# Performance work log

Measured on AMD Instinct MI355X. Metric: run time of the kernel, lower is better.

## Reference

```python
import jax, jax.numpy as jnp
import numpy as np

D_MODEL = 1024
D_FF = 2048
NA = 4
NB = 4
E = NA * NB
B = 2
S = 1024


def setup_inputs() -> dict:
    key = jax.random.key(0)
    ks = jax.random.split(key, 8)
    s = 0.02
    x = jax.random.normal(ks[0], (B, S, D_MODEL), dtype=jnp.float32)
    # stacked per-expert FFN params (torch Linear stored as [in, out] here)
    W1 = (jax.random.normal(ks[1], (E, D_MODEL, 2 * D_FF), dtype=jnp.float32) * s)
    b1 = jnp.zeros((E, 2 * D_FF), dtype=jnp.float32)
    W2 = (jax.random.normal(ks[2], (E, D_FF, D_MODEL), dtype=jnp.float32) * s)
    b2 = jnp.zeros((E, D_MODEL), dtype=jnp.float32)
    Wga = jax.random.normal(ks[3], (D_MODEL, NA), dtype=jnp.float32) * s
    bga = jnp.zeros((NA,), dtype=jnp.float32)
    Wgb = jax.random.normal(ks[4], (D_MODEL, NB), dtype=jnp.float32) * s
    bgb = jnp.zeros((NB,), dtype=jnp.float32)
    return {"x": x, "W1": W1, "b1": b1, "W2": W2, "b2": b2,
            "Wga": Wga, "bga": bga, "Wgb": Wgb, "bgb": bgb}


def reference(x, W1, b1, W2, b2, Wga, bga, Wgb, bgb):
    b, s, d = x.shape
    xf = x.reshape(b * s, d)                     # [T, d]
    probs_A = jax.nn.softmax(xf @ Wga + bga, axis=-1)   # [T, NA]
    probs_B = jax.nn.softmax(xf @ Wgb + bgb, axis=-1)   # [T, NB]
    idx_A = jnp.argmax(probs_A, axis=-1)
    idx_B = jnp.argmax(probs_B, axis=-1)
    oh_A = jax.nn.one_hot(idx_A, NA, dtype=xf.dtype)
    oh_B = jax.nn.one_hot(idx_B, NB, dtype=xf.dtype)
    aux_A = NA * jnp.sum(probs_A.mean(0) * oh_A.mean(0))
    aux_B = NB * jnp.sum(probs_B.mean(0) * oh_B.mean(0))
    total_aux = aux_A + aux_B

    # flattened Cartesian expert index per token
    e_idx = idx_A * NB + idx_B                   # [T]

    # run all experts densely, then select per token (vectorized dispatch)
    h = jnp.einsum('td,edf->etf', xf, W1) + b1[:, None, :]   # [E, T, 2*d_ff]
    a, g = jnp.split(h, 2, axis=-1)
    act = a * jax.nn.silu(g)                                  # [E, T, d_ff]
    y = jnp.einsum('etf,efd->etd', act, W2) + b2[:, None, :]  # [E, T, d]
    oh_E = jax.nn.one_hot(e_idx, E, dtype=xf.dtype)           # [T, E]
    out = jnp.einsum('te,etd->td', oh_E, y)                   # [T, d]
    return out.reshape(b, s, d), total_aux
```

## Files before the change

### kernel.cpp

```cpp
#include <hip/hip_runtime.h>
#include <cstdint>
#include <cstddef>

#define TOKENS 2048
#define DM 1024
#define DFF 2048
#define HC 4096
#define NE 16
#define BM 256

typedef __bf16 bf16x8 __attribute__((ext_vector_type(8)));
typedef float floatx4 __attribute__((ext_vector_type(4)));

static __device__ __forceinline__ unsigned short f2bf(float f) {
    union { float f; unsigned int u; } v; v.f = f;
    unsigned int r = v.u + 0x7fffu + ((v.u >> 16) & 1u);
    return (unsigned short)(r >> 16);
}

static __device__ __forceinline__ void lds_barrier() {
    asm volatile("s_waitcnt lgkmcnt(0)" ::: "memory");
    __builtin_amdgcn_s_barrier();
    __builtin_amdgcn_sched_barrier(0);
}

__global__ __launch_bounds__(256) void moe_gating(
    const float* __restrict__ x, const float* __restrict__ Wga, const float* __restrict__ bga,
    const float* __restrict__ Wgb, const float* __restrict__ bgb,
    float* __restrict__ probsA, float* __restrict__ probsB, int* __restrict__ e_idx)
{
    int wv = threadIdx.x >> 6, lane = threadIdx.x & 63;
    int t = blockIdx.x * 4 + wv;
    const float* xr = x + (size_t)t * DM;
    double aA[4] = {0.,0.,0.,0.}, aB[4] = {0.,0.,0.,0.};
    for (int k = lane; k < DM; k += 64) {
        double xv = (double)xr[k];
        float4 wa = *(const float4*)(Wga + k * 4);
        float4 wb = *(const float4*)(Wgb + k * 4);
        aA[0] += xv * wa.x; aA[1] += xv * wa.y; aA[2] += xv * wa.z; aA[3] += xv * wa.w;
        aB[0] += xv * wb.x; aB[1] += xv * wb.y; aB[2] += xv * wb.z; aB[3] += xv * wb.w;
    }
    #pragma unroll
    for (int off = 32; off >= 1; off >>= 1) {
        #pragma unroll
        for (int j = 0; j < 4; ++j) {
            aA[j] += __shfl_xor(aA[j], off);
            aB[j] += __shfl_xor(aB[j], off);
        }
    }
    if (lane == 0) {
        double lA[4], lB[4];
        #pragma unroll
        for (int j = 0; j < 4; ++j) {
            lA[j] = aA[j] + (double)bga[j];
            lB[j] = aB[j] + (double)bgb[j];
        }
        int ia = 0, ib = 0;
        #pragma unroll
        for (int j = 1; j < 4; ++j) {
            if (lA[j] > lA[ia]) ia = j;
            if (lB[j] > lB[ib]) ib = j;
        }
        double sA = 0., sB = 0., pA[4], pB[4];
        #pragma unroll
        for (int j = 0; j < 4; ++j) {
            pA[j] = exp(lA[j] - lA[ia]); sA += pA[j];
            pB[j] = exp(lB[j] - lB[ib]); sB += pB[j];
        }
        float4 oa, ob;
        oa.x = (float)(pA[0]/sA); oa.y = (float)(pA[1]/sA);
        oa.z = (float)(pA[2]/sA); oa.w = (float)(pA[3]/sA);
        ob.x = (float)(pB[0]/sB); ob.y = (float)(pB[1]/sB);
        ob.z = (float)(pB[2]/sB); ob.w = (float)(pB[3]/sB);
        *(float4*)(probsA + t * 4) = oa;
        *(float4*)(probsB + t * 4) = ob;
        e_idx[t] = ia * 4 + ib;
    }
}

__global__ __launch_bounds__(256) void moe_stats(
    const float* __restrict__ probsA, const float* __restrict__ probsB,
    const int* __restrict__ e_idx,
    int* __restrict__ countE, int* __restrict__ offsets, float* __restrict__ aux_out)
{
    __shared__ float sA[4], sB[4];
    __shared__ int cA[4], cB[4], cE[16];
    int tid = threadIdx.x;
    if (tid < 4) { sA[tid] = 0.f; sB[tid] = 0.f; cA[tid] = 0; cB[tid] = 0; }
    if (tid < 16) cE[tid] = 0;
    __syncthreads();
    float lA[4] = {0,0,0,0}, lB[4] = {0,0,0,0};
    for (int t = tid; t < TOKENS; t += 256) {
        float4 pa = *(const float4*)(probsA + t * 4);
        float4 pb = *(const float4*)(probsB + t * 4);
        lA[0] += pa.x; lA[1] += pa.y; lA[2] += pa.z; lA[3] += pa.w;
        lB[0] += pb.x; lB[1] += pb.y; lB[2] += pb.z; lB[3] += pb.w;
        int e = e_idx[t];
        atomicAdd(&cE[e], 1);
        atomicAdd(&cA[e >> 2], 1);
        atomicAdd(&cB[e & 3], 1);
    }
    #pragma unroll
    for (int j = 0; j < 4; ++j) {
        atomicAdd(&sA[j], lA[j]);
        atomicAdd(&sB[j], lB[j]);
    }
    __syncthreads();
    if (tid == 0) {
        int acc = 0;
        for (int e = 0; e < NE; ++e) { offsets[e] = acc; countE[e] = cE[e]; acc += cE[e]; }
        offsets[NE] = acc;
        float invT = 1.0f / (float)TOKENS;
        float auxA = 0.f, auxB = 0.f;
        for (int j = 0; j < 4; ++j) {
            auxA += (sA[j] * invT) * ((float)cA[j] * invT);
            auxB += (sB[j] * invT) * ((float)cB[j] * invT);
        }
        aux_out[0] = 4.0f * auxA + 4.0f * auxB;
    }
}

__global__ __launch_bounds__(256) void moe_slot(const int* __restrict__ e_idx,
                                                const int* __restrict__ offsets,
                                                int* __restrict__ cursor, int* __restrict__ perm)
{
    int t = blockIdx.x * 256 + threadIdx.x;
    int e = e_idx[t];
    int s = offsets[e] + atomicAdd(&cursor[e], 1);
    perm[s] = t;
}

__global__ __launch_bounds__(256) void moe_gather(const float* __restrict__ x,
                                                  const int* __restrict__ perm,
                                                  unsigned short* __restrict__ Xg)
{
    int s = blockIdx.x;
    int t = perm[s];
    int i = threadIdx.x * 4;
    float4 v = *(const float4*)(x + (size_t)t * DM + i);
    ushort4 o;
    o.x = f2bf(v.x); o.y = f2bf(v.y); o.z = f2bf(v.z); o.w = f2bf(v.w);
    *(ushort4*)(Xg + (size_t)s * DM + i) = o;
}

__global__ __launch_bounds__(512) void moe_ffn1(
    const unsigned short* __restrict__ Xg, const float* __restrict__ W1,
    const float* __restrict__ b1, const int* __restrict__ countE,
    const int* __restrict__ offsets, unsigned short* __restrict__ actbuf)
{
    int e = blockIdx.y;
    int cnt = countE[e];
    if (cnt == 0) return;
    int base = offsets[e];
    int n0 = blockIdx.x * 64;
    __shared__ __align__(16) unsigned short Xs[2 * BM * 40];
    int tid = threadIdx.x, wv = tid >> 6, lane = tid & 63;
    int quad = lane >> 4, l15 = lane & 15;
    int wvM = wv >> 2, wvN = wv & 3;
    const float* W1e = W1 + (size_t)e * DM * HC;
    int col = n0 + wvN * 16 + l15;
    const float* pa = W1e + col;
    const float* pg = W1e + DFF + col;
    float ba = b1[e * HC + col];
    float bg = b1[e * HC + DFF + col];
    int row = tid >> 2, kc = tid & 3;

    for (int m0 = 0; m0 < cnt; m0 += BM) {
        floatx4 acc[8][2];
        #pragma unroll
        for (int i = 0; i < 8; ++i) {
            acc[i][0] = floatx4{0.f,0.f,0.f,0.f};
            acc[i][1] = floatx4{0.f,0.f,0.f,0.f};
        }
        {
            uint4 av0 = {0u,0u,0u,0u}, av1 = {0u,0u,0u,0u};
            int ma = m0 + row, mb = m0 + row + 128;
            if (ma < cnt) av0 = *(const uint4*)(Xg + (size_t)(base + ma) * DM + kc * 8);
            if (mb < cnt) av1 = *(const uint4*)(Xg + (size_t)(base + mb) * DM + kc * 8);
            *(uint4*)(Xs + row * 40 + kc * 8) = av0;
            *(uint4*)(Xs + (row + 128) * 40 + kc * 8) = av1;
        }
        float curA[8], curG[8], nxtA[8], nxtG[8];
        {
            const float* qa = pa + (size_t)(quad * 8) * HC;
            const float* qg = pg + (size_t)(quad * 8) * HC;
            #pragma unroll
            for (int j = 0; j < 8; ++j) { curA[j] = qa[(size_t)j * HC]; curG[j] = qg[(size_t)j * HC]; }
        }
        lds_barrier();
        for (int ks = 0; ks < DM / 32; ++ks) {
            int buf = ks & 1;
            uint4 nv0 = {0u,0u,0u,0u}, nv1 = {0u,0u,0u,0u};
            bool more = (ks + 1 < DM / 32);
            if (more) {
                int k0n = (ks + 1) * 32;
                int ma = m0 + row, mb = m0 + row + 128;
                if (ma < cnt) nv0 = *(const uint4*)(Xg + (size_t)(base + ma) * DM + k0n + kc * 8);
                if (mb < cnt) nv1 = *(const uint4*)(Xg + (size_t)(base + mb) * DM + k0n + kc * 8);
                const float* qa = pa + (size_t)((ks + 1) * 32 + quad * 8) * HC;
                const float* qg = pg + (size_t)((ks + 1) * 32 + quad * 8) * HC;
                #pragma unroll
                for (int j = 0; j < 8; ++j) { nxtA[j] = qa[(size_t)j * HC]; nxtG[j] = qg[(size_t)j * HC]; }
            }
            bf16x8 af[8];
            #pragma unroll
            for (int i = 0; i < 8; ++i)
                af[i] = *(const bf16x8*)(Xs + buf * (BM * 40) + (wvM * 128 + i * 16 + l15) * 40 + quad * 8);
            bf16x8 fa, fg;
            #pragma unroll
            for (int j = 0; j < 8; ++j) { fa[j] = (__bf16)curA[j]; fg[j] = (__bf16)curG[j]; }
            #pragma unroll
            for (int i = 0; i < 8; ++i) {
                acc[i][0] = __builtin_amdgcn_mfma_f32_16x16x32_bf16(af[i], fa, acc[i][0], 0, 0, 0);
                acc[i][1] = __builtin_amdgcn_mfma_f32_16x16x32_bf16(af[i], fg, acc[i][1], 0, 0, 0);
            }
            if (more) {
                *(uint4*)(Xs + (buf ^ 1) * (BM * 40) + row * 40 + kc * 8) = nv0;
                *(uint4*)(Xs + (buf ^ 1) * (BM * 40) + (row + 128) * 40 + kc * 8) = nv1;
                #pragma unroll
                for (int j = 0; j < 8; ++j) { curA[j] = nxtA[j]; curG[j] = nxtG[j]; }
            }
            lds_barrier();
        }
        #pragma unroll
        for (int i = 0; i < 8; ++i) {
            #pragma unroll
            for (int r = 0; r < 4; ++r) {
                int mr = m0 + wvM * 128 + i * 16 + quad * 4 + r;
                if (mr < cnt) {
                    float a = acc[i][0][r] + ba;
                    float g = acc[i][1][r] + bg;
                    float sg = 1.0f / (1.0f + __expf(-g));
                    actbuf[(size_t)(base + mr) * DFF + col] = f2bf(a * (g * sg));
                }
            }
        }
    }
}

__global__ __launch_bounds__(512) void moe_ffn2(
    const unsigned short* __restrict__ actbuf, const float* __restrict__ W2,
    const float* __restrict__ b2, const int* __restrict__ countE,
    const int* __restrict__ offsets, const int* __restrict__ perm,
    float* __restrict__ out)
{
    int e = blockIdx.y;
    int cnt = countE[e];
    if (cnt == 0) return;
    int base = offsets[e];
    int n0 = blockIdx.x * 64;
    __shared__ __align__(16) unsigned short As[2 * BM * 40];
    int tid = threadIdx.x, wv = tid >> 6, lane = tid & 63;
    int quad = lane >> 4, l15 = lane & 15;
    int wvM = wv >> 2, wvN = wv & 3;
    const float* W2e = W2 + (size_t)e * DFF * DM;
    int col = n0 + wvN * 16 + l15;
    const float* pb = W2e + col;
    float bias = b2[e * DM + col];
    int row = tid >> 2, kc = tid & 3;

    for (int m0 = 0; m0 < cnt; m0 += BM) {
        floatx4 acc[8];
        #pragma unroll
        for (int i = 0; i < 8; ++i) acc[i] = floatx4{0.f,0.f,0.f,0.f};
        {
            uint4 av0 = {0u,0u,0u,0u}, av1 = {0u,0u,0u,0u};
            int ma = m0 + row, mb = m0 + row + 128;
            if (ma < cnt) av0 = *(const uint4*)(actbuf + (size_t)(base + ma) * DFF + kc * 8);
            if (mb < cnt) av1 = *(const uint4*)(actbuf + (size_t)(base + mb) * DFF + kc * 8);
            *(uint4*)(As + row * 40 + kc * 8) = av0;
            *(uint4*)(As + (row + 128) * 40 + kc * 8) = av1;
        }
        float curB[8], nxtB[8];
        {
            const float* qb = pb + (size_t)(quad * 8) * DM;
            #pragma unroll
            for (int j = 0; j < 8; ++j) curB[j] = qb[(size_t)j * DM];
        }
        lds_barrier();
        for (int ks = 0; ks < DFF / 32; ++ks) {
            int buf = ks & 1;
            uint4 nv0 = {0u,0u,0u,0u}, nv1 = {0u,0u,0u,0u};
            bool more = (ks + 1 < DFF / 32);
            if (more) {
                int k0n = (ks + 1) * 32;
                int ma = m0 + row, mb = m0 + row + 128;
                if (ma < cnt) nv0 = *(const uint4*)(actbuf + (size_t)(base + ma) * DFF + k0n + kc * 8);
                if (mb < cnt) nv1 = *(const uint4*)(actbuf + (size_t)(base + mb) * DFF + k0n + kc * 8);
                const float* qb = pb + (size_t)((ks + 1) * 32 + quad * 8) * DM;
                #pragma unroll
                for (int j = 0; j < 8; ++j) nxtB[j] = qb[(size_t)j * DM];
            }
            bf16x8 af[8];
            #pragma unroll
            for (int i = 0; i < 8; ++i)
                af[i] = *(const bf16x8*)(As + buf * (BM * 40) + (wvM * 128 + i * 16 + l15) * 40 + quad * 8);
            bf16x8 fb;
            #pragma unroll
            for (int j = 0; j < 8; ++j) fb[j] = (__bf16)curB[j];
            #pragma unroll
            for (int i = 0; i < 8; ++i)
                acc[i] = __builtin_amdgcn_mfma_f32_16x16x32_bf16(af[i], fb, acc[i], 0, 0, 0);
            if (more) {
                *(uint4*)(As + (buf ^ 1) * (BM * 40) + row * 40 + kc * 8) = nv0;
                *(uint4*)(As + (buf ^ 1) * (BM * 40) + (row + 128) * 40 + kc * 8) = nv1;
                #pragma unroll
                for (int j = 0; j < 8; ++j) curB[j] = nxtB[j];
            }
            lds_barrier();
        }
        #pragma unroll
        for (int i = 0; i < 8; ++i) {
            #pragma unroll
            for (int r = 0; r < 4; ++r) {
                int mr = m0 + wvM * 128 + i * 16 + quad * 4 + r;
                if (mr < cnt) {
                    int t = perm[base + mr];
                    out[(size_t)t * DM + col] = acc[i][r] + bias;
                }
            }
        }
    }
}

extern "C" void kernel_launch(void* const* d_in, const int* in_sizes, int n_in,
                              void* d_out, int out_size, void* d_ws, size_t ws_size,
                              hipStream_t stream)
{
    (void)in_sizes; (void)n_in; (void)out_size; (void)ws_size;
    const float* x   = (const float*)d_in[0];
    const float* W1  = (const float*)d_in[1];
    const float* b1  = (const float*)d_in[2];
    const float* W2  = (const float*)d_in[3];
    const float* b2  = (const float*)d_in[4];
    const float* Wga = (const float*)d_in[5];
    const float* bga = (const float*)d_in[6];
    const float* Wgb = (const float*)d_in[7];
    const float* bgb = (const float*)d_in[8];
    float* out = (float*)d_out;

    char* ws = (char*)d_ws;
    int*   countE  = (int*)(ws + 0);
    int*   cursor  = (int*)(ws + 64);
    int*   offsets = (int*)(ws + 256);
    int*   e_idx   = (int*)(ws + 512);
    int*   perm    = (int*)(ws + 8704);
    float* probsA  = (float*)(ws + 16896);
    float* probsB  = (float*)(ws + 49664);
    unsigned short* Xg     = (unsigned short*)(ws + 131072);
    unsigned short* actbuf = (unsigned short*)(ws + (size_t)8 * 1024 * 1024);

    hipMemsetAsync(ws, 0, 256, stream);
    moe_gating<<<TOKENS / 4, 256, 0, stream>>>(x, Wga, bga, Wgb, bgb,
                                               probsA, probsB, e_idx);
    moe_stats<<<1, 256, 0, stream>>>(probsA, probsB, e_idx, countE, offsets,
                                     out + (size_t)TOKENS * DM);
    moe_slot<<<TOKENS / 256, 256, 0, stream>>>(e_idx, offsets, cursor, perm);
    moe_gather<<<TOKENS, 256, 0, stream>>>(x, perm, Xg);
    moe_ffn1<<<dim3(DFF / 64, NE), 512, 0, stream>>>(Xg, W1, b1, countE, offsets, actbuf);
    moe_ffn2<<<dim3(DM / 64, NE), 512, 0, stream>>>(actbuf, W2, b2, countE, offsets, perm, out);
}
```

Baseline: 535.7 us.

## Retile expert FFN GEMMs to 192-row tiles with deeper A-prefetch and block swizzle

Both expert GEMM kernels now run 256-thread blocks, where each wave owns a 16-column strip and covers all 192 rows. Before, 512 threads split 256 rows across two wave groups. A activations are prefetched two k-steps ahead through register double buffers in an unrolled pair-step macro, and block IDs are remapped with an 8-way interleave that spreads experts across XCDs. The aim is fewer M-tiles for expert counts near 128 tokens, better latency hiding and occupancy of two blocks per CU. The cost is more accumulators per thread and higher register pressure.

```diff
diff --git a/kernel.cpp b/kernel.cpp
--- a/kernel.cpp
+++ b/kernel.cpp
@@ -7,7 +7,9 @@
 #define DFF 2048
 #define HC 4096
 #define NE 16
-#define BM 256
+#define BM 192
+#define NBX1 32
+#define NBX2 16
 
 typedef __bf16 bf16x8 __attribute__((ext_vector_type(8)));
 typedef float floatx4 __attribute__((ext_vector_type(4)));
@@ -143,22 +145,63 @@
     *(ushort4*)(Xg + (size_t)s * DM + i) = o;
 }
 
-__global__ __launch_bounds__(512) void moe_ffn1(
+#define NS1 (DM / 32)
+
+#define FFN1_STEP(ksv, RW, RL) {                                               \
+    int buf_ = (ksv) & 1;                                                      \
+    if ((ksv) + 1 < NS1) {                                                     \
+        _Pragma("unroll")                                                      \
+        for (int p = 0; p < 3; ++p)                                            \
+            *(uint4*)(Xs + (buf_ ^ 1) * (BM * 40) + (row + p * 64) * 40 + kc * 8) = RW[p]; \
+    }                                                                          \
+    if ((ksv) + 2 < NS1) {                                                     \
+        int k0n_ = ((ksv) + 2) * 32;                                           \
+        _Pragma("unroll")                                                      \
+        for (int p = 0; p < 3; ++p) {                                          \
+            int m_ = m0 + row + p * 64;                                        \
+            RL[p].x = 0u; RL[p].y = 0u; RL[p].z = 0u; RL[p].w = 0u;            \
+            if (m_ < cnt) RL[p] = *(const uint4*)(Xg + (size_t)(base + m_) * DM + k0n_ + kc * 8); \
+        }                                                                      \
+    }                                                                          \
+    if ((ksv) + 1 < NS1) {                                                     \
+        const float* qa_ = pa + (size_t)(((ksv) + 1) * 32 + quad * 8) * HC;    \
+        const float* qg_ = pg + (size_t)(((ksv) + 1) * 32 + quad * 8) * HC;    \
+        _Pragma("unroll")                                                      \
+        for (int j = 0; j < 8; ++j) { nxtA[j] = qa_[(size_t)j * HC]; nxtG[j] = qg_[(size_t)j * HC]; } \
+    }                                                                          \
+    bf16x8 fa_, fg_;                                                           \
+    _Pragma("unroll")                                                          \
+    for (int j = 0; j < 8; ++j) { fa_[j] = (__bf16)curA[j]; fg_[j] = (__bf16)curG[j]; } \
+    _Pragma("unroll")                                                          \
+    for (int i = 0; i < 12; ++i) {                                             \
+        bf16x8 af_ = *(const bf16x8*)(Xs + buf_ * (BM * 40) + (i * 16 + l15) * 40 + quad * 8); \
+        acc[i][0] = __builtin_amdgcn_mfma_f32_16x16x32_bf16(af_, fa_, acc[i][0], 0, 0, 0); \
+        acc[i][1] = __builtin_amdgcn_mfma_f32_16x16x32_bf16(af_, fg_, acc[i][1], 0, 0, 0); \
+    }                                                                          \
+    if ((ksv) + 1 < NS1) {                                                     \
+        _Pragma("unroll")                                                      \
+        for (int j = 0; j < 8; ++j) { curA[j] = nxtA[j]; curG[j] = nxtG[j]; }  \
+    }                                                                          \
+    lds_barrier();                                                             \
+}
+
+__global__ __launch_bounds__(256, 2) void moe_ffn1(
     const unsigned short* __restrict__ Xg, const float* __restrict__ W1,
     const float* __restrict__ b1, const int* __restrict__ countE,
     const int* __restrict__ offsets, unsigned short* __restrict__ actbuf)
 {
-    int e = blockIdx.y;
+    int id = blockIdx.y * NBX1 + blockIdx.x;
+    int lid = (id & 7) * ((NBX1 * NE) >> 3) + (id >> 3);
+    int e = lid >> 5;
+    int n0 = (lid & 31) * 64;
     int cnt = countE[e];
     if (cnt == 0) return;
     int base = offsets[e];
-    int n0 = blockIdx.x * 64;
     __shared__ __align__(16) unsigned short Xs[2 * BM * 40];
     int tid = threadIdx.x, wv = tid >> 6, lane = tid & 63;
     int quad = lane >> 4, l15 = lane & 15;
-    int wvM = wv >> 2, wvN = wv & 3;
     const float* W1e = W1 + (size_t)e * DM * HC;
-    int col = n0 + wvN * 16 + l15;
+    int col = n0 + wv * 16 + l15;
     const float* pa = W1e + col;
     const float* pg = W1e + DFF + col;
     float ba = b1[e * HC + col];
@@ -166,19 +209,25 @@
     int row = tid >> 2, kc = tid & 3;
 
     for (int m0 = 0; m0 < cnt; m0 += BM) {
-        floatx4 acc[8][2];
-        #pragma unroll
-        for (int i = 0; i < 8; ++i) {
+        floatx4 acc[12][2];
+        #pragma unroll
+        for (int i = 0; i < 12; ++i) {
             acc[i][0] = floatx4{0.f,0.f,0.f,0.f};
             acc[i][1] = floatx4{0.f,0.f,0.f,0.f};
         }
-        {
-            uint4 av0 = {0u,0u,0u,0u}, av1 = {0u,0u,0u,0u};
-            int ma = m0 + row, mb = m0 + row + 128;
-            if (ma < cnt) av0 = *(const uint4*)(Xg + (size_t)(base + ma) * DM + kc * 8);
-            if (mb < cnt) av1 = *(const uint4*)(Xg + (size_t)(base + mb) * DM + kc * 8);
-            *(uint4*)(Xs + row * 40 + kc * 8) = av0;
-            *(uint4*)(Xs + (row + 128) * 40 + kc * 8) = av1;
+        uint4 R0[3], R1[3];
+        #pragma unroll
+        for (int p = 0; p < 3; ++p) {
+            int m = m0 + row + p * 64;
+            uint4 v; v.x = 0u; v.y = 0u; v.z = 0u; v.w = 0u;
+            if (m < cnt) v = *(const uint4*)(Xg + (size_t)(base + m) * DM + kc * 8);
+            *(uint4*)(Xs + (row + p * 64) * 40 + kc * 8) = v;
+        }
+        #pragma unroll
+        for (int p = 0; p < 3; ++p) {
+            int m = m0 + row + p * 64;
+            R0[p].x = 0u; R0[p].y = 0u; R0[p].z = 0u; R0[p].w = 0u;
+            if (m < cnt) R0[p] = *(const uint4*)(Xg + (size_t)(base + m) * DM + 32 + kc * 8);
         }
         float curA[8], curG[8], nxtA[8], nxtG[8];
         {
@@ -188,45 +237,15 @@
             for (int j = 0; j < 8; ++j) { curA[j] = qa[(size_t)j * HC]; curG[j] = qg[(size_t)j * HC]; }
         }
         lds_barrier();
-        for (int ks = 0; ks < DM / 32; ++ks) {
-            int buf = ks & 1;
-            uint4 nv0 = {0u,0u,0u,0u}, nv1 = {0u,0u,0u,0u};
-            bool more = (ks + 1 < DM / 32);
-            if (more) {
-                int k0n = (ks + 1) * 32;
-                int ma = m0 + row, mb = m0 + row + 128;
-                if (ma < cnt) nv0 = *(const uint4*)(Xg + (size_t)(base + ma) * DM + k0n + kc * 8);
-                if (mb < cnt) nv1 = *(const uint4*)(Xg + (size_t)(base + mb) * DM + k0n + kc * 8);
-                const float* qa = pa + (size_t)((ks + 1) * 32 + quad * 8) * HC;
-                const float* qg = pg + (size_t)((ks + 1) * 32 + quad * 8) * HC;
-                #pragma unroll
-                for (int j = 0; j < 8; ++j) { nxtA[j] = qa[(size_t)j * HC]; nxtG[j] = qg[(size_t)j * HC]; }
-            }
-            bf16x8 af[8];
-            #pragma unroll
-            for (int i = 0; i < 8; ++i)
-                af[i] = *(const bf16x8*)(Xs + buf * (BM * 40) + (wvM * 128 + i * 16 + l15) * 40 + quad * 8);
-            bf16x8 fa, fg;
-            #pragma unroll
-            for (int j = 0; j < 8; ++j) { fa[j] = (__bf16)curA[j]; fg[j] = (__bf16)curG[j]; }
-            #pragma unroll
-            for (int i = 0; i < 8; ++i) {
-                acc[i][0] = __builtin_amdgcn_mfma_f32_16x16x32_bf16(af[i], fa, acc[i][0], 0, 0, 0);
-                acc[i][1] = __builtin_amdgcn_mfma_f32_16x16x32_bf16(af[i], fg, acc[i][1], 0, 0, 0);
-            }
-            if (more) {
-                *(uint4*)(Xs + (buf ^ 1) * (BM * 40) + row * 40 + kc * 8) = nv0;
-                *(uint4*)(Xs + (buf ^ 1) * (BM * 40) + (row + 128) * 40 + kc * 8) = nv1;
-                #pragma unroll
-                for (int j = 0; j < 8; ++j) { curA[j] = nxtA[j]; curG[j] = nxtG[j]; }
-            }
-            lds_barrier();
-        }
-        #pragma unroll
-        for (int i = 0; i < 8; ++i) {
+        for (int ks = 0; ks < NS1; ks += 2) {
+            FFN1_STEP(ks, R0, R1);
+            FFN1_STEP(ks + 1, R1, R0);
+        }
+        #pragma unroll
+        for (int i = 0; i < 12; ++i) {
             #pragma unroll
             for (int r = 0; r < 4; ++r) {
-                int mr = m0 + wvM * 128 + i * 16 + quad * 4 + r;
+                int mr = m0 + i * 16 + quad * 4 + r;
                 if (mr < cnt) {
                     float a = acc[i][0][r] + ba;
                     float g = acc[i][1][r] + bg;
@@ -238,38 +257,83 @@
     }
 }
 
-__global__ __launch_bounds__(512) void moe_ffn2(
+#define NS2 (DFF / 32)
+
+#define FFN2_STEP(ksv, RW, RL) {                                               \
+    int buf_ = (ksv) & 1;                                                      \
+    if ((ksv) + 1 < NS2) {                                                     \
+        _Pragma("unroll")                                                      \
+        for (int p = 0; p < 3; ++p)                                            \
+            *(uint4*)(As + (buf_ ^ 1) * (BM * 40) + (row + p * 64) * 40 + kc * 8) = RW[p]; \
+    }                                                                          \
+    if ((ksv) + 2 < NS2) {                                                     \
+        int k0n_ = ((ksv) + 2) * 32;                                           \
+        _Pragma("unroll")                                                      \
+        for (int p = 0; p < 3; ++p) {                                          \
+            int m_ = m0 + row + p * 64;                                        \
+            RL[p].x = 0u; RL[p].y = 0u; RL[p].z = 0u; RL[p].w = 0u;            \
+            if (m_ < cnt) RL[p] = *(const uint4*)(actbuf + (size_t)(base + m_) * DFF + k0n_ + kc * 8); \
+        }                                                                      \
+    }                                                                          \
+    if ((ksv) + 1 < NS2) {                                                     \
+        const float* qb_ = pb + (size_t)(((ksv) + 1) * 32 + quad * 8) * DM;    \
+        _Pragma("unroll")                                                      \
+        for (int j = 0; j < 8; ++j) nxtB[j] = qb_[(size_t)j * DM];             \
+    }                                                                          \
+    bf16x8 fb_;                                                                \
+    _Pragma("unroll")                                                          \
+    for (int j = 0; j < 8; ++j) fb_[j] = (__bf16)curB[j];                      \
+    _Pragma("unroll")                                                          \
+    for (int i = 0; i < 12; ++i) {                                             \
+        bf16x8 af_ = *(const bf16x8*)(As + buf_ * (BM * 40) + (i * 16 + l15) * 40 + quad * 8); \
+        acc[i] = __builtin_amdgcn_mfma_f32_16x16x32_bf16(af_, fb_, acc[i], 0, 0, 0); \
+    }                                                                          \
+    if ((ksv) + 1 < NS2) {                                                     \
+        _Pragma("unroll")                                                      \
+        for (int j = 0; j < 8; ++j) curB[j] = nxtB[j];                         \
+    }                                                                          \
+    lds_barrier();                                                             \
+}
+
+__global__ __launch_bounds__(256, 2) void moe_ffn2(
     const unsigned short* __restrict__ actbuf, const float* __restrict__ W2,
     const float* __restrict__ b2, const int* __restrict__ countE,
     const int* __restrict__ offsets, const int* __restrict__ perm,
     float* __restrict__ out)
 {
-    int e = blockIdx.y;
+    int id = blockIdx.y * NBX2 + blockIdx.x;
+    int lid = (id & 7) * ((NBX2 * NE) >> 3) + (id >> 3);
+    int e = lid >> 4;
+    int n0 = (lid & 15) * 64;
     int cnt = countE[e];
     if (cnt == 0) return;
     int base = offsets[e];
-    int n0 = blockIdx.x * 64;
     __shared__ __align__(16) unsigned short As[2 * BM * 40];
     int tid = threadIdx.x, wv = tid >> 6, lane = tid & 63;
     int quad = lane >> 4, l15 = lane & 15;
-    int wvM = wv >> 2, wvN = wv & 3;
     const float* W2e = W2 + (size_t)e * DFF * DM;
-    int col = n0 + wvN * 16 + l15;
+    int col = n0 + wv * 16 + l15;
     const float* pb = W2e + col;
     float bias = b2[e * DM + col];
     int row = tid >> 2, kc = tid & 3;
 
     for (int m0 = 0; m0 < cnt; m0 += BM) {
-        floatx4 acc[8];
-        #pragma unroll
-        for (int i = 0; i < 8; ++i) acc[i] = floatx4{0.f,0.f,0.f,0.f};
-        {
-            uint4 av0 = {0u,0u,0u,0u}, av1 = {0u,0u,0u,0u};
-            int ma = m0 + row, mb = m0 + row + 128;
-            if (ma < cnt) av0 = *(const uint4*)(actbuf + (size_t)(base + ma) * DFF + kc * 8);
-            if (mb < cnt) av1 = *(const uint4*)(actbuf + (size_t)(base + mb) * DFF + kc * 8);
-            *(uint4*)(As + row * 40 + kc * 8) = av0;
-            *(uint4*)(As + (row + 128) * 40 + kc * 8) = av1;
+        floatx4 acc[12];
+        #pragma unroll
+        for (int i = 0; i < 12; ++i) acc[i] = floatx4{0.f,0.f,0.f,0.f};
+        uint4 R0[3], R1[3];
+        #pragma unroll
+        for (int p = 0; p < 3; ++p) {
+            int m = m0 + row + p * 64;
+            uint4 v; v.x = 0u; v.y = 0u; v.z = 0u; v.w = 0u;
+            if (m < cnt) v = *(const uint4*)(actbuf + (size_t)(base + m) * DFF + kc * 8);
+            *(uint4*)(As + (row + p * 64) * 40 + kc * 8) = v;
+        }
+        #pragma unroll
+        for (int p = 0; p < 3; ++p) {
+            int m = m0 + row + p * 64;
+            R0[p].x = 0u; R0[p].y = 0u; R0[p].z = 0u; R0[p].w = 0u;
+            if (m < cnt) R0[p] = *(const uint4*)(actbuf + (size_t)(base + m) * DFF + 32 + kc * 8);
         }
         float curB[8], nxtB[8];
         {
@@ -278,42 +342,15 @@
             for (int j = 0; j < 8; ++j) curB[j] = qb[(size_t)j * DM];
         }
         lds_barrier();
-        for (int ks = 0; ks < DFF / 32; ++ks) {
-            int buf = ks & 1;
-            uint4 nv0 = {0u,0u,0u,0u}, nv1 = {0u,0u,0u,0u};
-            bool more = (ks + 1 < DFF / 32);
-            if (more) {
-                int k0n = (ks + 1) * 32;
-                int ma = m0 + row, mb = m0 + row + 128;
-                if (ma < cnt) nv0 = *(const uint4*)(actbuf + (size_t)(base + ma) * DFF + k0n + kc * 8);
-                if (mb < cnt) nv1 = *(const uint4*)(actbuf + (size_t)(base + mb) * DFF + k0n + kc * 8);
-                const float* qb = pb + (size_t)((ks + 1) * 32 + quad * 8) * DM;
-                #pragma unroll
-                for (int j = 0; j < 8; ++j) nxtB[j] = qb[(size_t)j * DM];
-            }
-            bf16x8 af[8];
-            #pragma unroll
-            for (int i = 0; i < 8; ++i)
-                af[i] = *(const bf16x8*)(As + buf * (BM * 40) + (wvM * 128 + i * 16 + l15) * 40 + quad * 8);
-            bf16x8 fb;
-            #pragma unroll
-            for (int j = 0; j < 8; ++j) fb[j] = (__bf16)curB[j];
-            #pragma unroll
-            for (int i = 0; i < 8; ++i)
-                acc[i] = __builtin_amdgcn_mfma_f32_16x16x32_bf16(af[i], fb, acc[i], 0, 0, 0);
-            if (more) {
-                *(uint4*)(As + (buf ^ 1) * (BM * 40) + row * 40 + kc * 8) = nv0;
-                *(uint4*)(As + (buf ^ 1) * (BM * 40) + (row + 128) * 40 + kc * 8) = nv1;
-                #pragma unroll
-                for (int j = 0; j < 8; ++j) curB[j] = nxtB[j];
-            }
-            lds_barrier();
-        }
-        #pragma unroll
-        for (int i = 0; i < 8; ++i) {
+        for (int ks = 0; ks < NS2; ks += 2) {
+            FFN2_STEP(ks, R0, R1);
+            FFN2_STEP(ks + 1, R1, R0);
+        }
+        #pragma unroll
+        for (int i = 0; i < 12; ++i) {
             #pragma unroll
             for (int r = 0; r < 4; ++r) {
-                int mr = m0 + wvM * 128 + i * 16 + quad * 4 + r;
+                int mr = m0 + i * 16 + quad * 4 + r;
                 if (mr < cnt) {
                     int t = perm[base + mr];
                     out[(size_t)t * DM + col] = acc[i][r] + bias;
@@ -357,6 +394,6 @@
                                      out + (size_t)TOKENS * DM);
     moe_slot<<<TOKENS / 256, 256, 0, stream>>>(e_idx, offsets, cursor, perm);
     moe_gather<<<TOKENS, 256, 0, stream>>>(x, perm, Xg);
-    moe_ffn1<<<dim3(DFF / 64, NE), 512, 0, stream>>>(Xg, W1, b1, countE, offsets, actbuf);
-    moe_ffn2<<<dim3(DM / 64, NE), 512, 0, stream>>>(actbuf, W2, b2, countE, offsets, perm, out);
-}
+    moe_ffn1<<<dim3(NBX1, NE), 256, 0, stream>>>(Xg, W1, b1, countE, offsets, actbuf);
+    moe_ffn2<<<dim3(NBX2, NE), 256, 0, stream>>>(actbuf, W2, b2, countE, offsets, perm, out);
+}
```

Measured after the change: 540.3 us. No clear change (+0.9%).
